# Kernel tuning notes

Measured on AMD Instinct MI355X. Metric: run time of the kernel, lower is better.

Reference implementation:

```python
import jax, jax.numpy as jnp
import numpy as np


def setup_inputs() -> dict:
    key = jax.random.key(0)
    ks = jax.random.split(key, 6)
    N, C, T, V = 32, 64, 128, 25
    F = C * T * V  # 204800
    H = 256
    E = 4
    stdv0 = 1.0 / np.sqrt(F)
    stdv1 = 1.0 / np.sqrt(H)
    stdvA = 1.0 / np.sqrt(V)
    return {
        "x": jax.random.normal(ks[0], (N, C, T, V), dtype=jnp.float32),
        "W0": jax.random.uniform(ks[1], (F, H), jnp.float32, -stdv0, stdv0),
        "b0": jnp.zeros((H,), jnp.float32),
        "W1": jax.random.uniform(ks[2], (H, H), jnp.float32, -stdv1, stdv1),
        "b1": jnp.zeros((H,), jnp.float32),
        "W2": jax.random.uniform(ks[3], (H, E), jnp.float32, -stdv1, stdv1),
        "b2": jnp.zeros((E,), jnp.float32),
        "A": jax.random.uniform(ks[4], (E, T, V, V), jnp.float32, -stdvA, stdvA),
    }


def reference(x, W0, b0, W1, b1, W2, b2, A):
    N = x.shape[0]
    # Gating MLP (dropout treated as identity / eval mode)
    g = x.reshape(N, -1)                      # [N, C*T*V]
    h = jax.nn.elu(g @ W0 + b0)               # [N, 256]
    h = jax.nn.elu(h @ W1 + b1)               # [N, 256]
    logits = h @ W2 + b2                      # [N, 4]
    w = jax.nn.softmax(logits, axis=1)        # [N, 4]
    # Mixture of adjacency experts: AS[n,t,v,w] = sum_e w[n,e] * A[e,t,v,w]
    AS = jnp.einsum('ne,etvw->ntvw', w, A)    # [N, T, V, V]
    # Batched graph convolution
    out = jnp.einsum('nctv,ntvw->nctw', x, AS)
    return out
```

## Files before the change

### kernel.cpp

```cpp
#include <hip/hip_runtime.h>
#include <math.h>

#define Nn 32
#define Cc 64
#define Tt 128
#define Vv 25
#define Kk 204800
#define Hh 256
#define Ee 4
#define KC 256
#define KB 16
#define NSTEP (KC / KB)
#define NBLK_A 800

__device__ __forceinline__ float elu1(float v) { return v > 0.0f ? v : expm1f(v); }

typedef const __attribute__((address_space(1))) void* gvp;
typedef __attribute__((address_space(3))) void* lvp;
__device__ __forceinline__ void gl_lds16(const void* g, void* l) {
  __builtin_amdgcn_global_load_lds((gvp)g, (lvp)l, 16, 0, 0);
}

__global__ __launch_bounds__(256) void kA(const float* __restrict__ x,
                                          const float* __restrict__ W0,
                                          float* __restrict__ partials) {
  __shared__ float xs[Nn][KC];
  __shared__ float wbuf[2][KB][Hh];
  const int tid  = threadIdx.x;
  const int lane = tid & 63;
  const int wv   = tid >> 6;
  const int b  = blockIdx.x;
  const int k0 = b * KC;

  for (int r = wv; r < Nn; r += 4)
    gl_lds16(x + (size_t)r * Kk + k0 + lane * 4, &xs[r][0]);
  for (int r = wv; r < KB; r += 4)
    gl_lds16(W0 + (size_t)(k0 + r) * Hh + lane * 4, &wbuf[0][r][0]);
  __syncthreads();

  const int hg = tid & 31;
  const int np = tid >> 5;
  const int h0 = hg * 8;
  const int n0 = np * 4;

  float acc[4][8];
  #pragma unroll
  for (int i = 0; i < 4; ++i)
    #pragma unroll
    for (int c = 0; c < 8; ++c) acc[i][c] = 0.0f;

  for (int step = 0; step < NSTEP; ++step) {
    const int cur = step & 1;
    if (step + 1 < NSTEP) {
      const int kb = (step + 1) * KB;
      for (int r = wv; r < KB; r += 4)
        gl_lds16(W0 + (size_t)(k0 + kb + r) * Hh + lane * 4, &wbuf[cur ^ 1][r][0]);
    }
    const int kbase = step * KB;
    #pragma unroll
    for (int kk = 0; kk < KB; kk += 4) {
      float4 xv[4];
      #pragma unroll
      for (int i = 0; i < 4; ++i)
        xv[i] = *(const float4*)&xs[n0 + i][kbase + kk];
      #pragma unroll
      for (int u = 0; u < 4; ++u) {
        const float* wp = &wbuf[cur][kk + u][h0];
        float4 wa = *(const float4*)(wp);
        float4 wb = *(const float4*)(wp + 4);
        #pragma unroll
        for (int i = 0; i < 4; ++i) {
          float xu = (u == 0) ? xv[i].x : (u == 1) ? xv[i].y : (u == 2) ? xv[i].z : xv[i].w;
          acc[i][0] = fmaf(xu, wa.x, acc[i][0]);
          acc[i][1] = fmaf(xu, wa.y, acc[i][1]);
          acc[i][2] = fmaf(xu, wa.z, acc[i][2]);
          acc[i][3] = fmaf(xu, wa.w, acc[i][3]);
          acc[i][4] = fmaf(xu, wb.x, acc[i][4]);
          acc[i][5] = fmaf(xu, wb.y, acc[i][5]);
          acc[i][6] = fmaf(xu, wb.z, acc[i][6]);
          acc[i][7] = fmaf(xu, wb.w, acc[i][7]);
        }
      }
    }
    __syncthreads();
  }

  #pragma unroll
  for (int i = 0; i < 4; ++i) {
    float* pp = partials + ((size_t)(b * Nn + n0 + i) << 8) + h0;
    *(float4*)(pp)     = make_float4(acc[i][0], acc[i][1], acc[i][2], acc[i][3]);
    *(float4*)(pp + 4) = make_float4(acc[i][4], acc[i][5], acc[i][6], acc[i][7]);
  }
}

__global__ __launch_bounds__(256) void kB1(const float* __restrict__ partials,
                                           const float* __restrict__ b0,
                                           float* __restrict__ hb) {
  const int n  = blockIdx.x >> 3;
  const int hc = blockIdx.x & 7;
  const int tid = threadIdx.x;
  const int hl = tid & 31;
  const int bsub = tid >> 5;
  const int h = hc * 32 + hl;
  float s = 0.0f;
  for (int j = 0; j < 100; ++j) {
    int b = bsub * 100 + j;
    s += partials[((size_t)(b * Nn + n) << 8) + h];
  }
  __shared__ float red[8][32];
  red[bsub][hl] = s;
  __syncthreads();
  if (tid < 32) {
    float tot = 0.0f;
    #pragma unroll
    for (int sI = 0; sI < 8; ++sI) tot += red[sI][tid];
    int hh = hc * 32 + tid;
    hb[n * Hh + hh] = elu1(tot + b0[hh]);
  }
}

__global__ __launch_bounds__(256) void kB2(const float* __restrict__ hb,
                                           const float* __restrict__ W1,
                                           const float* __restrict__ b1,
                                           const float* __restrict__ W2,
                                           const float* __restrict__ b2,
                                           float* __restrict__ wgt) {
  const int n = blockIdx.x;
  const int tid = threadIdx.x;
  __shared__ float hbs[Hh];
  hbs[tid] = hb[n * Hh + tid];
  __syncthreads();
  float s = b1[tid];
  for (int j = 0; j < Hh; ++j) s = fmaf(hbs[j], W1[j * Hh + tid], s);
  float h2 = elu1(s);
  float le[Ee];
  #pragma unroll
  for (int e = 0; e < Ee; ++e) le[e] = h2 * W2[tid * Ee + e];
  __shared__ float red[Ee][4];
  const int lane = tid & 63;
  const int wid  = tid >> 6;
  #pragma unroll
  for (int e = 0; e < Ee; ++e) {
    float v = le[e];
    for (int off = 32; off > 0; off >>= 1) v += __shfl_down(v, off, 64);
    if (lane == 0) red[e][wid] = v;
  }
  __syncthreads();
  if (tid == 0) {
    float lg[Ee];
    float m = -1e30f;
    #pragma unroll
    for (int e = 0; e < Ee; ++e) {
      lg[e] = red[e][0] + red[e][1] + red[e][2] + red[e][3] + b2[e];
      m = fmaxf(m, lg[e]);
    }
    float den = 0.0f;
    #pragma unroll
    for (int e = 0; e < Ee; ++e) { lg[e] = expf(lg[e] - m); den += lg[e]; }
    float inv = 1.0f / den;
    #pragma unroll
    for (int e = 0; e < Ee; ++e) wgt[n * Ee + e] = lg[e] * inv;
  }
}

#define ASW 28
#define XTS 68
__global__ __launch_bounds__(256) void kC(const float* __restrict__ x,
                                          const float* __restrict__ A,
                                          const float* __restrict__ wgt,
                                          float* __restrict__ out) {
  const int blk = blockIdx.x;
  const int n  = blk >> 6;
  const int tp = blk & 63;
  const int tid = threadIdx.x;
  const int tsub = tid >> 7;
  const int tl = tid & 127;
  const int t = tp * 2 + tsub;

  __shared__ float AS[2][Vv][ASW];
  __shared__ float xT[2][Vv][XTS];

  float wv[Ee];
  #pragma unroll
  for (int e = 0; e < Ee; ++e) wv[e] = wgt[n * Ee + e];

  for (int idx = tl; idx < Vv * ASW; idx += 128) {
    int v = idx / ASW;
    int w = idx - v * ASW;
    float s = 0.0f;
    if (w < Vv) {
      #pragma unroll
      for (int e = 0; e < Ee; ++e)
        s = fmaf(wv[e], A[((size_t)(e * Tt + t) * Vv + v) * Vv + w], s);
    }
    AS[tsub][v][w] = s;
  }
  const float* xb = x + (size_t)n * (Cc * Tt * Vv) + (size_t)t * Vv;
  for (int idx = tl; idx < Cc * Vv; idx += 128) {
    int c = idx / Vv;
    int v = idx - c * Vv;
    xT[tsub][v][c] = xb[(size_t)c * (Tt * Vv) + v];
  }
  __syncthreads();

  const int ct = tl & 15;
  const int wq = tl >> 4;
  if (wq < 7) {
    const int c0 = ct * 4;
    const int w0 = wq * 4;
    float acc[4][4];
    #pragma unroll
    for (int i = 0; i < 4; ++i)
      #pragma unroll
      for (int j = 0; j < 4; ++j) acc[i][j] = 0.0f;
    #pragma unroll 5
    for (int v = 0; v < Vv; ++v) {
      float4 a4 = *(const float4*)&AS[tsub][v][w0];
      float4 x4 = *(const float4*)&xT[tsub][v][c0];
      const float xr[4] = {x4.x, x4.y, x4.z, x4.w};
      const float ar[4] = {a4.x, a4.y, a4.z, a4.w};
      #pragma unroll
      for (int i = 0; i < 4; ++i)
        #pragma unroll
        for (int j = 0; j < 4; ++j)
          acc[i][j] = fmaf(xr[i], ar[j], acc[i][j]);
    }
    #pragma unroll
    for (int i = 0; i < 4; ++i) {
      int c = c0 + i;
      float* ob = out + ((size_t)(n * Cc + c) * Tt + t) * Vv;
      #pragma unroll
      for (int j = 0; j < 4; ++j) {
        int w = w0 + j;
        if (w < Vv) ob[w] = acc[i][j];
      }
    }
  }
}

extern "C" void kernel_launch(void* const* d_in, const int* in_sizes, int n_in,
                              void* d_out, int out_size, void* d_ws, size_t ws_size,
                              hipStream_t stream) {
  const float* x  = (const float*)d_in[0];
  const float* W0 = (const float*)d_in[1];
  const float* b0 = (const float*)d_in[2];
  const float* W1 = (const float*)d_in[3];
  const float* b1 = (const float*)d_in[4];
  const float* W2 = (const float*)d_in[5];
  const float* b2 = (const float*)d_in[6];
  const float* A  = (const float*)d_in[7];
  float* out = (float*)d_out;

  float* partials = (float*)d_ws;
  float* hb  = partials + (size_t)NBLK_A * Nn * Hh;
  float* wgt = hb + Nn * Hh;

  kA <<<NBLK_A,  256, 0, stream>>>(x, W0, partials);
  kB1<<<256,     256, 0, stream>>>(partials, b0, hb);
  kB2<<<Nn,      256, 0, stream>>>(hb, W1, b1, W2, b2, wgt);
  kC <<<Nn * 64, 256, 0, stream>>>(x, A, wgt, out);
}
```

Baseline: 379.7 us.

## Give each wave a private W0 column slice with 4-deep barrier-free prefetch ring

In the first GEMV kernel, each wavefront now owns a 64-column slice of W0 and streams it through its own 4-slot LDS ring via direct global-to-LDS loads, synchronized only with per-wave vmcnt waits instead of block-wide barriers every step. The x tile is loaded through registers into an XOR-swizzled LDS layout to avoid bank conflicts, and the K step shrinks to 4 rows with three stages of prefetch in flight. This aims to remove barrier stalls and keep more W0 traffic outstanding, at the cost of reliance on hand-placed waitcnt counts and smaller transfers per step.

Result: slower. 414.7 us (+9.2%).

```diff
diff --git a/kernel.cpp b/kernel.cpp
--- a/kernel.cpp
+++ b/kernel.cpp
@@ -9,7 +9,7 @@
 #define Hh 256
 #define Ee 4
 #define KC 256
-#define KB 16
+#define KB 4
 #define NSTEP (KC / KB)
 #define NBLK_A 800
 
@@ -25,23 +25,33 @@
                                           const float* __restrict__ W0,
                                           float* __restrict__ partials) {
   __shared__ float xs[Nn][KC];
-  __shared__ float wbuf[2][KB][Hh];
+  __shared__ float wsl[4][4][KB][64];
   const int tid  = threadIdx.x;
   const int lane = tid & 63;
   const int wv   = tid >> 6;
   const int b  = blockIdx.x;
   const int k0 = b * KC;
 
-  for (int r = wv; r < Nn; r += 4)
-    gl_lds16(x + (size_t)r * Kk + k0 + lane * 4, &xs[r][0]);
-  for (int r = wv; r < KB; r += 4)
-    gl_lds16(W0 + (size_t)(k0 + r) * Hh + lane * 4, &wbuf[0][r][0]);
-  __syncthreads();
-
-  const int hg = tid & 31;
-  const int np = tid >> 5;
-  const int h0 = hg * 8;
-  const int n0 = np * 4;
+  for (int i = tid; i < Nn * (KC / 4); i += 256) {
+    int r  = i >> 6;
+    int c4 = i & 63;
+    float4 v = *(const float4*)(x + (size_t)r * Kk + k0 + c4 * 4);
+    *(float4*)&xs[r][(c4 ^ (r >> 2)) * 4] = v;
+  }
+  asm volatile("s_waitcnt vmcnt(0)" ::: "memory");
+
+  const int hbase = wv * 64;
+  const size_t gking = (size_t)(lane >> 4) * Hh + hbase + (lane & 15) * 4;
+  #pragma unroll
+  for (int s = 0; s < 3; ++s)
+    gl_lds16(W0 + (size_t)(k0 + s * KB) * Hh + gking, &wsl[wv][s][0][0]);
+
+  asm volatile("s_waitcnt lgkmcnt(0)" ::: "memory");
+  __syncthreads();
+
+  const int j8 = lane >> 3;
+  const int n0 = j8 * 4;
+  const int h0 = (lane & 7) * 8;
 
   float acc[4][8];
   #pragma unroll
@@ -50,44 +60,48 @@
     for (int c = 0; c < 8; ++c) acc[i][c] = 0.0f;
 
   for (int step = 0; step < NSTEP; ++step) {
-    const int cur = step & 1;
-    if (step + 1 < NSTEP) {
-      const int kb = (step + 1) * KB;
-      for (int r = wv; r < KB; r += 4)
-        gl_lds16(W0 + (size_t)(k0 + kb + r) * Hh + lane * 4, &wbuf[cur ^ 1][r][0]);
-    }
-    const int kbase = step * KB;
-    #pragma unroll
-    for (int kk = 0; kk < KB; kk += 4) {
-      float4 xv[4];
-      #pragma unroll
-      for (int i = 0; i < 4; ++i)
-        xv[i] = *(const float4*)&xs[n0 + i][kbase + kk];
-      #pragma unroll
-      for (int u = 0; u < 4; ++u) {
-        const float* wp = &wbuf[cur][kk + u][h0];
-        float4 wa = *(const float4*)(wp);
-        float4 wb = *(const float4*)(wp + 4);
-        #pragma unroll
-        for (int i = 0; i < 4; ++i) {
-          float xu = (u == 0) ? xv[i].x : (u == 1) ? xv[i].y : (u == 2) ? xv[i].z : xv[i].w;
-          acc[i][0] = fmaf(xu, wa.x, acc[i][0]);
-          acc[i][1] = fmaf(xu, wa.y, acc[i][1]);
-          acc[i][2] = fmaf(xu, wa.z, acc[i][2]);
-          acc[i][3] = fmaf(xu, wa.w, acc[i][3]);
-          acc[i][4] = fmaf(xu, wb.x, acc[i][4]);
-          acc[i][5] = fmaf(xu, wb.y, acc[i][5]);
-          acc[i][6] = fmaf(xu, wb.z, acc[i][6]);
-          acc[i][7] = fmaf(xu, wb.w, acc[i][7]);
-        }
+    if (step < NSTEP - 2) {
+      asm volatile("s_waitcnt vmcnt(2)" ::: "memory");
+    } else if (step == NSTEP - 2) {
+      asm volatile("s_waitcnt vmcnt(1)" ::: "memory");
+    } else {
+      asm volatile("s_waitcnt vmcnt(0)" ::: "memory");
+    }
+    __builtin_amdgcn_sched_barrier(0);
+
+    if (step + 3 < NSTEP)
+      gl_lds16(W0 + (size_t)(k0 + (step + 3) * KB) * Hh + gking,
+               &wsl[wv][(step + 3) & 3][0][0]);
+
+    const int slot = step & 3;
+    const int xcol = (step ^ j8) * 4;
+    float4 xv[4];
+    #pragma unroll
+    for (int i = 0; i < 4; ++i)
+      xv[i] = *(const float4*)&xs[n0 + i][xcol];
+    #pragma unroll
+    for (int u = 0; u < 4; ++u) {
+      const float* wp = &wsl[wv][slot][u][h0];
+      float4 wa = *(const float4*)(wp);
+      float4 wb = *(const float4*)(wp + 4);
+      #pragma unroll
+      for (int i = 0; i < 4; ++i) {
+        float xu = (u == 0) ? xv[i].x : (u == 1) ? xv[i].y : (u == 2) ? xv[i].z : xv[i].w;
+        acc[i][0] = fmaf(xu, wa.x, acc[i][0]);
+        acc[i][1] = fmaf(xu, wa.y, acc[i][1]);
+        acc[i][2] = fmaf(xu, wa.z, acc[i][2]);
+        acc[i][3] = fmaf(xu, wa.w, acc[i][3]);
+        acc[i][4] = fmaf(xu, wb.x, acc[i][4]);
+        acc[i][5] = fmaf(xu, wb.y, acc[i][5]);
+        acc[i][6] = fmaf(xu, wb.z, acc[i][6]);
+        acc[i][7] = fmaf(xu, wb.w, acc[i][7]);
       }
     }
-    __syncthreads();
   }
 
   #pragma unroll
   for (int i = 0; i < 4; ++i) {
-    float* pp = partials + ((size_t)(b * Nn + n0 + i) << 8) + h0;
+    float* pp = partials + ((size_t)(b * Nn + n0 + i) << 8) + hbase + h0;
     *(float4*)(pp)     = make_float4(acc[i][0], acc[i][1], acc[i][2], acc[i][3]);
     *(float4*)(pp + 4) = make_float4(acc[i][4], acc[i][5], acc[i][6], acc[i][7]);
   }
```

## Stream W0 directly from global into registers and transpose x tile in LDS

Applied to the files above, without the earlier changes.

Reworks the big GEMV-like kernel kA. Before, W0 was staged through double-buffered LDS using global_load_lds. Now each thread reads its W0 row slice straight from global memory as float4, and only x is kept in LDS, stored transposed with padding so one float4 read returns 8 batch values per k. The aim is to drop the LDS traffic and barriers for W0, cut LDS use, and raise occupancy via launch_bounds(256,4). The tradeoff is that latency hiding for W0 now depends on the unrolled loop and on occupancy rather than explicit prefetch, and the transposed scalar writes into LDS may cause bank conflicts.

New measurement: 390.0 us. 1.03x slower.

```diff
diff --git a/kernel.cpp b/kernel.cpp
--- a/kernel.cpp
+++ b/kernel.cpp
@@ -9,87 +9,62 @@
 #define Hh 256
 #define Ee 4
 #define KC 256
-#define KB 16
-#define NSTEP (KC / KB)
+#define XPAD 36
 #define NBLK_A 800
 
 __device__ __forceinline__ float elu1(float v) { return v > 0.0f ? v : expm1f(v); }
 
-typedef const __attribute__((address_space(1))) void* gvp;
-typedef __attribute__((address_space(3))) void* lvp;
-__device__ __forceinline__ void gl_lds16(const void* g, void* l) {
-  __builtin_amdgcn_global_load_lds((gvp)g, (lvp)l, 16, 0, 0);
-}
-
-__global__ __launch_bounds__(256) void kA(const float* __restrict__ x,
-                                          const float* __restrict__ W0,
-                                          float* __restrict__ partials) {
-  __shared__ float xs[Nn][KC];
-  __shared__ float wbuf[2][KB][Hh];
+__global__ __launch_bounds__(256, 4) void kA(const float* __restrict__ x,
+                                             const float* __restrict__ W0,
+                                             float* __restrict__ partials) {
+  __shared__ float xsT[KC][XPAD];
   const int tid  = threadIdx.x;
   const int lane = tid & 63;
   const int wv   = tid >> 6;
   const int b  = blockIdx.x;
   const int k0 = b * KC;
 
-  for (int r = wv; r < Nn; r += 4)
-    gl_lds16(x + (size_t)r * Kk + k0 + lane * 4, &xs[r][0]);
-  for (int r = wv; r < KB; r += 4)
-    gl_lds16(W0 + (size_t)(k0 + r) * Hh + lane * 4, &wbuf[0][r][0]);
-  __syncthreads();
-
-  const int hg = tid & 31;
-  const int np = tid >> 5;
-  const int h0 = hg * 8;
-  const int n0 = np * 4;
-
-  float acc[4][8];
-  #pragma unroll
-  for (int i = 0; i < 4; ++i)
-    #pragma unroll
-    for (int c = 0; c < 8; ++c) acc[i][c] = 0.0f;
-
-  for (int step = 0; step < NSTEP; ++step) {
-    const int cur = step & 1;
-    if (step + 1 < NSTEP) {
-      const int kb = (step + 1) * KB;
-      for (int r = wv; r < KB; r += 4)
-        gl_lds16(W0 + (size_t)(k0 + kb + r) * Hh + lane * 4, &wbuf[cur ^ 1][r][0]);
-    }
-    const int kbase = step * KB;
-    #pragma unroll
-    for (int kk = 0; kk < KB; kk += 4) {
-      float4 xv[4];
-      #pragma unroll
-      for (int i = 0; i < 4; ++i)
-        xv[i] = *(const float4*)&xs[n0 + i][kbase + kk];
-      #pragma unroll
-      for (int u = 0; u < 4; ++u) {
-        const float* wp = &wbuf[cur][kk + u][h0];
-        float4 wa = *(const float4*)(wp);
-        float4 wb = *(const float4*)(wp + 4);
-        #pragma unroll
-        for (int i = 0; i < 4; ++i) {
-          float xu = (u == 0) ? xv[i].x : (u == 1) ? xv[i].y : (u == 2) ? xv[i].z : xv[i].w;
-          acc[i][0] = fmaf(xu, wa.x, acc[i][0]);
-          acc[i][1] = fmaf(xu, wa.y, acc[i][1]);
-          acc[i][2] = fmaf(xu, wa.z, acc[i][2]);
-          acc[i][3] = fmaf(xu, wa.w, acc[i][3]);
-          acc[i][4] = fmaf(xu, wb.x, acc[i][4]);
-          acc[i][5] = fmaf(xu, wb.y, acc[i][5]);
-          acc[i][6] = fmaf(xu, wb.z, acc[i][6]);
-          acc[i][7] = fmaf(xu, wb.w, acc[i][7]);
-        }
-      }
-    }
-    __syncthreads();
-  }
-
-  #pragma unroll
-  for (int i = 0; i < 4; ++i) {
-    float* pp = partials + ((size_t)(b * Nn + n0 + i) << 8) + h0;
-    *(float4*)(pp)     = make_float4(acc[i][0], acc[i][1], acc[i][2], acc[i][3]);
-    *(float4*)(pp + 4) = make_float4(acc[i][4], acc[i][5], acc[i][6], acc[i][7]);
+  for (int i = tid; i < Nn * (KC / 4); i += 256) {
+    int n  = i >> 6;
+    int c4 = i & 63;
+    float4 v = *(const float4*)(x + (size_t)n * Kk + k0 + c4 * 4);
+    xsT[c4 * 4 + 0][n] = v.x;
+    xsT[c4 * 4 + 1][n] = v.y;
+    xsT[c4 * 4 + 2][n] = v.z;
+    xsT[c4 * 4 + 3][n] = v.w;
+  }
+  __syncthreads();
+
+  const int n0 = wv * 8;
+  const int h4 = lane * 4;
+
+  float acc[8][4];
+  #pragma unroll
+  for (int j = 0; j < 8; ++j)
+    #pragma unroll
+    for (int c = 0; c < 4; ++c) acc[j][c] = 0.0f;
+
+  const float* wp = W0 + (size_t)k0 * Hh + h4;
+  #pragma unroll 8
+  for (int k = 0; k < KC; ++k) {
+    float4 w = *(const float4*)(wp);
+    wp += Hh;
+    float4 xa = *(const float4*)&xsT[k][n0];
+    float4 xb = *(const float4*)&xsT[k][n0 + 4];
+    const float xr[8] = {xa.x, xa.y, xa.z, xa.w, xb.x, xb.y, xb.z, xb.w};
+    #pragma unroll
+    for (int j = 0; j < 8; ++j) {
+      acc[j][0] = fmaf(xr[j], w.x, acc[j][0]);
+      acc[j][1] = fmaf(xr[j], w.y, acc[j][1]);
+      acc[j][2] = fmaf(xr[j], w.z, acc[j][2]);
+      acc[j][3] = fmaf(xr[j], w.w, acc[j][3]);
+    }
+  }
+
+  #pragma unroll
+  for (int j = 0; j < 8; ++j) {
+    float* pp = partials + ((size_t)(b * Nn + n0 + j) << 8) + h4;
+    *(float4*)(pp) = make_float4(acc[j][0], acc[j][1], acc[j][2], acc[j][3]);
   }
 }
 
```
